# Performance work log

Measured on AMD Instinct MI355X. Metric: run time of the kernel, lower is better.

## Reference

```python
import jax, jax.numpy as jnp
import numpy as np
import math

N_EMBD = 768
N_HEAD = 12
B, T = 4, 1024


def setup_inputs() -> dict:
    key = jax.random.key(0)
    ks = jax.random.split(key, 12)
    s = 0.02
    d = N_EMBD
    inp = {
        'x': jax.random.normal(ks[0], (B, T, d), dtype=jnp.float32),
        'refractory_state': jax.random.uniform(ks[1], (B, T), dtype=jnp.float32),
        'ln1_w': jnp.ones((d,), jnp.float32),
        'ln1_b': jnp.zeros((d,), jnp.float32),
        'c_attn_w': jax.random.normal(ks[2], (d, 3 * d), dtype=jnp.float32) * s,
        'c_attn_b': jnp.zeros((3 * d,), jnp.float32),
        'c_proj_w': jax.random.normal(ks[3], (d, d), dtype=jnp.float32) * s,
        'c_proj_b': jnp.zeros((d,), jnp.float32),
        'threshold': jnp.full((N_HEAD,), 0.01, jnp.float32),
        'leak': jnp.full((N_HEAD,), 2.0, jnp.float32),
        'steepness': jnp.full((N_HEAD,), 2.0, jnp.float32),
        'refractory_strength': jnp.full((N_HEAD,), -2.0, jnp.float32),
        'cross_layer_weight': jnp.full((N_HEAD,), -2.0, jnp.float32),
        'ln2_w': jnp.ones((d,), jnp.float32),
        'ln2_b': jnp.zeros((d,), jnp.float32),
        'fc_w': jax.random.normal(ks[4], (d, 4 * d), dtype=jnp.float32) * s,
        'fc_b': jnp.zeros((4 * d,), jnp.float32),
        'proj_w': jax.random.normal(ks[5], (4 * d, d), dtype=jnp.float32) * s,
        'proj_b': jnp.zeros((d,), jnp.float32),
    }
    return inp


def _layer_norm(x, w, b, eps=1e-5):
    m = jnp.mean(x, axis=-1, keepdims=True)
    v = jnp.var(x, axis=-1, keepdims=True)
    return (x - m) * jax.lax.rsqrt(v + eps) * w + b


def _per_head(p):
    # [H] -> [1, H, 1, 1]
    return p.reshape(1, -1, 1, 1)


def ember_block(x, refractory_state, ln1_w, ln1_b, c_attn_w, c_attn_b,
                c_proj_w, c_proj_b, threshold, leak, steepness,
                refractory_strength, cross_layer_weight,
                ln2_w, ln2_b, fc_w, fc_b, proj_w, proj_b):
    Bx, Tx, C = x.shape
    hd = C // N_HEAD

    h = _layer_norm(x, ln1_w, ln1_b)
    qkv = h @ c_attn_w + c_attn_b
    q, k, v = jnp.split(qkv, 3, axis=-1)
    # [B, T, C] -> [B, H, T, hd]
    q = q.reshape(Bx, Tx, N_HEAD, hd).transpose(0, 2, 1, 3)
    k = k.reshape(Bx, Tx, N_HEAD, hd).transpose(0, 2, 1, 3)
    v = v.reshape(Bx, Tx, N_HEAD, hd).transpose(0, 2, 1, 3)

    att = jnp.einsum('bhqd,bhkd->bhqk', q, k) * (1.0 / math.sqrt(hd))
    causal = jnp.tril(jnp.ones((Tx, Tx), dtype=bool))
    att = jnp.where(causal, att, -jnp.inf)
    att_probs = jax.nn.softmax(att, axis=-1)

    # per-head LIF modulation with refractory dynamics
    thr = jnp.abs(_per_head(threshold)) * 0.1
    lk = jax.nn.sigmoid(_per_head(leak))
    stp = jax.nn.softplus(_per_head(steepness))

    column_load = att_probs.mean(axis=-2, keepdims=True)  # [B,H,1,T]
    ref_strength = jax.nn.softplus(_per_head(refractory_strength))
    eff_thr = thr + ref_strength * column_load
    cross_w = jax.nn.sigmoid(_per_head(cross_layer_weight))
    prev_load = refractory_state[:, None, None, :]  # [B,1,1,T]
    eff_thr = eff_thr + cross_w * prev_load

    fire_mask = jax.nn.sigmoid(stp * (att_probs - eff_thr))
    lif_weights = fire_mask + lk * (1.0 - fire_mask)
    modulated = att_probs * lif_weights
    modulated = modulated / (modulated.sum(axis=-1, keepdims=True) + 1e-8)
    new_refractory = modulated.mean(axis=1).mean(axis=-2)  # [B,T]

    y = jnp.einsum('bhqk,bhkd->bhqd', modulated, v)
    y = y.transpose(0, 2, 1, 3).reshape(Bx, Tx, C)
    y = y @ c_proj_w + c_proj_b
    x = x + y

    # MLP
    h2 = _layer_norm(x, ln2_w, ln2_b)
    h2 = jax.nn.gelu(h2 @ fc_w + fc_b, approximate=False)
    h2 = h2 @ proj_w + proj_b
    x = x + h2
    return x, new_refractory


def reference(x, refractory_state, ln1_w, ln1_b, c_attn_w, c_attn_b,
              c_proj_w, c_proj_b, threshold, leak, steepness,
              refractory_strength, cross_layer_weight,
              ln2_w, ln2_b, fc_w, fc_b, proj_w, proj_b):
    return ember_block(x, refractory_state, ln1_w, ln1_b, c_attn_w, c_attn_b,
                       c_proj_w, c_proj_b, threshold, leak, steepness,
                       refractory_strength, cross_layer_weight,
                       ln2_w, ln2_b, fc_w, fc_b, proj_w, proj_b)
```

## Files before the change

kernel.cpp:

```cpp
#include <hip/hip_runtime.h>
#include <hip/hip_bf16.h>
#include <math.h>

typedef unsigned short ushort;
typedef __attribute__((ext_vector_type(8))) unsigned short ushort8;
typedef __attribute__((ext_vector_type(8))) short s16x8;
typedef __attribute__((ext_vector_type(4))) float f32x4;

constexpr int NE = 768;
constexpr int NH = 12;
constexpr int HD = 64;
constexpr int Bc = 4;
constexpr int Tc = 1024;
constexpr int BT = Bc * Tc;

__device__ __forceinline__ ushort f2bf(float f) {
    __hip_bfloat16 h = __float2bfloat16(f);
    return *reinterpret_cast<ushort*>(&h);
}
__device__ __forceinline__ float bf2f(ushort u) {
    return __uint_as_float(((unsigned)u) << 16);
}
__device__ __forceinline__ float softplus_f(float x) {
    return (x > 20.f) ? x : log1pf(__expf(x));
}
__device__ __forceinline__ float rcp_f(float x) {
#if __has_builtin(__builtin_amdgcn_rcpf)
    return __builtin_amdgcn_rcpf(x);
#else
    return 1.f / x;
#endif
}
__device__ __forceinline__ void gload16(const void* g, void* l) {
    __builtin_amdgcn_global_load_lds((const __attribute__((address_space(1))) void*)g,
                                     (__attribute__((address_space(3))) void*)l, 16, 0, 0);
}

__global__ __launch_bounds__(256) void ln_kernel(const float* __restrict__ x,
                                                 const float* __restrict__ w,
                                                 const float* __restrict__ b,
                                                 ushort* __restrict__ out) {
    int row = blockIdx.x;
    const float* xr = x + (size_t)row * NE;
    int t = threadIdx.x;
    float v0 = xr[t], v1 = xr[t + 256], v2 = xr[t + 512];
    __shared__ float red[256], red2[256];
    red[t] = v0 + v1 + v2;
    red2[t] = v0 * v0 + v1 * v1 + v2 * v2;
    __syncthreads();
    for (int o = 128; o > 0; o >>= 1) {
        if (t < o) { red[t] += red[t + o]; red2[t] += red2[t + o]; }
        __syncthreads();
    }
    float mean = red[0] * (1.0f / NE);
    float var = red2[0] * (1.0f / NE) - mean * mean;
    float rs = rsqrtf(var + 1e-5f);
    ushort* orow = out + (size_t)row * NE;
    orow[t]       = f2bf((v0 - mean) * rs * w[t]       + b[t]);
    orow[t + 256] = f2bf((v1 - mean) * rs * w[t + 256] + b[t + 256]);
    orow[t + 512] = f2bf((v2 - mean) * rs * w[t + 512] + b[t + 512]);
}

__global__ __launch_bounds__(256) void wconvert(const float* __restrict__ W,
                                                ushort* __restrict__ Wt, int K, int N) {
    __shared__ float t[32][33];
    int n0 = blockIdx.x * 32, k0 = blockIdx.y * 32;
    int c = threadIdx.x & 31, r4 = threadIdx.x >> 5;
#pragma unroll
    for (int i = 0; i < 4; ++i) {
        int r = r4 + i * 8;
        t[r][c] = W[(size_t)(k0 + r) * N + n0 + c];
    }
    __syncthreads();
#pragma unroll
    for (int i = 0; i < 4; ++i) {
        int r = r4 + i * 8;
        Wt[(size_t)(n0 + r) * K + k0 + c] = f2bf(t[c][r]);
    }
}

template <int BM, int BN, int OUT_MODE, int ACT, bool RES>
__global__ __launch_bounds__(256) void mfma_gemm(
    const ushort* __restrict__ A, const ushort* __restrict__ Bt,
    const float* __restrict__ bias, const float* __restrict__ residual,
    float* __restrict__ Cf, ushort* __restrict__ Cb,
    ushort* __restrict__ Qo, ushort* __restrict__ Ko, ushort* __restrict__ Vo,
    int M, int N, int K, int NBX) {
    constexpr int NF = (BM == 128) ? 4 : 2;
    constexpr int MF = (BM == 64 && BN == 64) ? 2 : 4;
    constexpr int WN = BN / (NF * 16);
    constexpr int APASS = BM / 32, BPASS = BN / 32;
    __shared__ __align__(16) ushort As[BM * 64];
    __shared__ __align__(16) ushort Bs[BN * 64];
    int tid = threadIdx.x;
    int lane = tid & 63;
    int nb = gridDim.x;
    int lin = blockIdx.x;
    int nl = (lin & 7) * (nb >> 3) + (lin >> 3);
    int bx = nl % NBX, by = nl / NBX;
    int m0 = by * BM, n0 = bx * BN;
    int wave = tid >> 6;
    int wr = wave / WN, wc = wave % WN;
    f32x4 acc[MF][NF] = {};
    int srow = tid >> 3;
    int scol = (tid & 7) ^ (srow & 7);
    const ushort* ga = A + (size_t)(m0 + srow) * K + scol * 8;
    const ushort* gb = Bt + (size_t)(n0 + srow) * K + scol * 8;
    char* lA = (char*)As + tid * 16;
    char* lB = (char*)Bs + tid * 16;
    int fr = lane & 15, g = lane >> 4;
    unsigned swz = (unsigned)((fr & 7) << 4);
    const char* abase = (const char*)As + (wr * (MF * 16) + fr) * 128;
    const char* bbase = (const char*)Bs + (wc * (NF * 16) + fr) * 128;
    for (int k0 = 0; k0 < K; k0 += 64) {
#pragma unroll
        for (int p = 0; p < APASS; ++p)
            gload16(ga + (size_t)(p * 32) * K + k0, lA + p * 4096);
#pragma unroll
        for (int p = 0; p < BPASS; ++p)
            gload16(gb + (size_t)(p * 32) * K + k0, lB + p * 4096);
        __syncthreads();
#pragma unroll
        for (int ks = 0; ks < 2; ++ks) {
            unsigned o = ((unsigned)(g * 16 + ks * 64)) ^ swz;
            s16x8 af[MF], bf[NF];
#pragma unroll
            for (int i = 0; i < MF; ++i) af[i] = *(const s16x8*)(abase + i * 2048 + o);
#pragma unroll
            for (int i = 0; i < NF; ++i) bf[i] = *(const s16x8*)(bbase + i * 2048 + o);
#pragma unroll
            for (int mi = 0; mi < MF; ++mi)
#pragma unroll
                for (int ni = 0; ni < NF; ++ni)
                    acc[mi][ni] = __builtin_amdgcn_mfma_f32_16x16x32_bf16(af[mi], bf[ni], acc[mi][ni], 0, 0, 0);
        }
        __syncthreads();
    }
#pragma unroll
    for (int mi = 0; mi < MF; ++mi) {
#pragma unroll
        for (int ni = 0; ni < NF; ++ni) {
#pragma unroll
            for (int j = 0; j < 4; ++j) {
                int row = m0 + wr * (MF * 16) + mi * 16 + g * 4 + j;
                int col = n0 + wc * (NF * 16) + ni * 16 + fr;
                float v = acc[mi][ni][j] + bias[col];
                if (ACT == 1) v = 0.5f * v * (1.0f + erff(v * 0.70710678118654752f));
                if (RES) v += residual[(size_t)row * N + col];
                if (OUT_MODE == 0) {
                    Cf[(size_t)row * N + col] = v;
                } else if (OUT_MODE == 1) {
                    Cb[(size_t)row * N + col] = f2bf(v);
                } else {
                    int which = col >= 1536 ? 2 : (col >= 768 ? 1 : 0);
                    int rem = col - which * 768;
                    int hh = rem >> 6, d = rem & 63;
                    int b_ = row >> 10, t_ = row & 1023;
                    if (which == 2)
                        Vo[((size_t)(b_ * NH + hh) * HD + d) * Tc + t_] = f2bf(v);
                    else {
                        ushort* dst = which == 0 ? Qo : Ko;
                        dst[((size_t)(b_ * NH + hh) * Tc + t_) * HD + d] = f2bf(v);
                    }
                }
            }
        }
    }
}


__global__ __launch_bounds__(256) void attn_P(
    const ushort* __restrict__ Qp, const ushort* __restrict__ Kp,
    ushort* __restrict__ Pbuf, float* __restrict__ denom, float* __restrict__ colsum) {
    int beta = blockIdx.x;
    int tq = 63 - beta / 48;
    int bh = beta % 48;
    int tid = threadIdx.x;
    int w = tid >> 6, lane = tid & 63, qlane = lane & 15, g = lane >> 4;
    __shared__ ushort plds[4][16][48];
    __shared__ float cs[1056];
    __shared__ float dden[4][16];
    __shared__ float dinvL[16];
    int nst = (tq + 2) >> 1;
    int base = nst >> 2, rem = nst & 3;
    int slo = w * base + (w < rem ? w : rem);
    int shi = slo + base + (w < rem ? 1 : 0);
    int kmaxc = (tq + 1) * 16;
    for (int i = tid; i < 1056; i += 256) cs[i] = 0.f;
    const ushort* Qb = Qp + (size_t)bh * Tc * HD;
    const ushort* Kb = Kp + (size_t)bh * Tc * HD;
    const ushort* qr = Qb + (size_t)(tq * 16 + qlane) * HD + g * 8;
    s16x8 qf0 = *(const s16x8*)qr;
    s16x8 qf1 = *(const s16x8*)(qr + 32);
    ushort* panel = Pbuf + ((size_t)bh * 1056 + (unsigned)(((tq + 1) * (tq + 1)) >> 2)) * 512;
    int q = tq * 16 + qlane;
    float dpart = 0.f;
    for (int s = slo; s < shi; ++s) {
        int kt0 = 2 * s, kt1 = 2 * s + 1;
        {
            const ushort* kr = Kb + (size_t)(kt0 * 16 + qlane) * HD + g * 8;
            s16x8 kf0 = *(const s16x8*)kr;
            s16x8 kf1 = *(const s16x8*)(kr + 32);
            f32x4 z = {0.f, 0.f, 0.f, 0.f};
            z = __builtin_amdgcn_mfma_f32_16x16x32_bf16(kf0, qf0, z, 0, 0, 0);
            z = __builtin_amdgcn_mfma_f32_16x16x32_bf16(kf1, qf1, z, 0, 0, 0);
#pragma unroll
            for (int j = 0; j < 4; ++j) {
                int key = kt0 * 16 + g * 4 + j;
                float p = (key <= q) ? __expf(z[j] * 0.125f - 8.f) : 0.f;
                dpart += p;
                plds[w][qlane][g * 4 + j] = f2bf(p);
            }
        }
        if (kt1 <= tq) {
            const ushort* kr = Kb + (size_t)(kt1 * 16 + qlane) * HD + g * 8;
            s16x8 kf0 = *(const s16x8*)kr;
            s16x8 kf1 = *(const s16x8*)(kr + 32);
            f32x4 z = {0.f, 0.f, 0.f, 0.f};
            z = __builtin_amdgcn_mfma_f32_16x16x32_bf16(kf0, qf0, z, 0, 0, 0);
            z = __builtin_amdgcn_mfma_f32_16x16x32_bf16(kf1, qf1, z, 0, 0, 0);
#pragma unroll
            for (int j = 0; j < 4; ++j) {
                int key = kt1 * 16 + g * 4 + j;
                float p = (key <= q) ? __expf(z[j] * 0.125f - 8.f) : 0.f;
                dpart += p;
                plds[w][qlane][16 + g * 4 + j] = f2bf(p);
            }
        } else {
#pragma unroll
            for (int j = 0; j < 4; ++j) plds[w][qlane][16 + g * 4 + j] = 0;
        }
        s16x8 pa = *(const s16x8*)&plds[w][qlane][g * 8];
        *(s16x8*)(panel + (size_t)s * 512 + lane * 8) = pa;
    }
    dpart += __shfl_xor(dpart, 16);
    dpart += __shfl_xor(dpart, 32);
    if (lane < 16) dden[w][lane] = dpart;
    __syncthreads();
    if (tid < 16) {
        float d = dden[0][tid] + dden[1][tid] + dden[2][tid] + dden[3][tid];
        denom[(size_t)bh * Tc + tq * 16 + tid] = d;
        dinvL[tid] = rcp_f(d);
    }
    __syncthreads();
    float dinvq = dinvL[qlane];
    for (int s = slo; s < shi; ++s) {
        s16x8 v8 = *(const s16x8*)(panel + (size_t)s * 512 + lane * 8);
        int k0 = s * 32 + g * 8;
#pragma unroll
        for (int j = 0; j < 8; ++j) {
            float r = bf2f((ushort)v8[j]) * dinvq;
            r += __shfl_xor(r, 1);
            r += __shfl_xor(r, 2);
            r += __shfl_xor(r, 4);
            r += __shfl_xor(r, 8);
            if (qlane == 0) cs[k0 + j] += r;
        }
    }
    __syncthreads();
    for (int i = tid; i < kmaxc; i += 256)
        atomicAdd(&colsum[(size_t)bh * Tc + i], cs[i]);
}

__global__ __launch_bounds__(256) void attn_CD(
    const ushort* __restrict__ Pbuf, const ushort* __restrict__ Vt,
    const float* __restrict__ denom, const float* __restrict__ colsum,
    const float* __restrict__ refr_in,
    const float* __restrict__ threshold, const float* __restrict__ leak,
    const float* __restrict__ steepness, const float* __restrict__ refr_strength,
    const float* __restrict__ cross_w,
    ushort* __restrict__ ybuf, float* __restrict__ refr_out) {
    int beta = blockIdx.x;
    int tq = 63 - beta / 48;
    int bh = beta % 48;
    int b = bh / NH, h = bh - b * NH;
    int tid = threadIdx.x;
    int w = tid >> 6, lane = tid & 63, qlane = lane & 15, g = lane >> 4;
    __shared__ float eff[1056];
    __shared__ float cs[1056];
    __shared__ float msum[4][16];
    __shared__ float minvL[16];
    __shared__ float ylds[16][64];
    int nst = (tq + 2) >> 1;
    int base = nst >> 2, rem = nst & 3;
    int slo = w * base + (w < rem ? w : rem);
    int shi = slo + base + (w < rem ? 1 : 0);
    int kmaxc = (tq + 1) * 16;
    float thr = fabsf(threshold[h]) * 0.1f;
    float lk = 1.f / (1.f + __expf(-leak[h]));
    float lk1m = 1.f - lk;
    float stp = softplus_f(steepness[h]);
    float rfs = softplus_f(refr_strength[h]);
    float crw = 1.f / (1.f + __expf(-cross_w[h]));
    for (int i = tid; i < 1056; i += 256) {
        eff[i] = (i < kmaxc)
                     ? thr + rfs * (colsum[(size_t)bh * Tc + i] * (1.f / 1024.f))
                           + crw * refr_in[(size_t)b * Tc + i]
                     : 0.f;
        cs[i] = 0.f;
    }
    for (int i = tid; i < 1024; i += 256) ((float*)ylds)[i] = 0.f;
    float dinvq = rcp_f(denom[(size_t)bh * Tc + tq * 16 + qlane]);
    __syncthreads();
    const ushort* panel =
        Pbuf + ((size_t)bh * 1056 + (unsigned)(((tq + 1) * (tq + 1)) >> 2)) * 512;
    float msp = 0.f;
#pragma unroll 2
    for (int s = slo; s < shi; ++s) {
        s16x8 v8 = *(const s16x8*)(panel + (size_t)s * 512 + lane * 8);
        int k0 = s * 32 + g * 8;
#pragma unroll
        for (int j = 0; j < 8; ++j) {
            float p = bf2f((ushort)v8[j]) * dinvq;
            float fire = rcp_f(1.f + __expf(-stp * (p - eff[k0 + j])));
            msp += p * (lk + lk1m * fire);
        }
    }
    msp += __shfl_xor(msp, 16);
    msp += __shfl_xor(msp, 32);
    if (lane < 16) msum[w][lane] = msp;
    __syncthreads();
    if (tid < 16)
        minvL[tid] = rcp_f(msum[0][tid] + msum[1][tid] + msum[2][tid] + msum[3][tid] + 1e-8f);
    __syncthreads();
    float minvq = minvL[qlane];
    const ushort* Vh = Vt + (size_t)bh * HD * Tc;
    f32x4 accY[4] = {};
    for (int s = slo; s < shi; ++s) {
        s16x8 v8 = *(const s16x8*)(panel + (size_t)s * 512 + lane * 8);
        int k0 = s * 32 + g * 8;
        s16x8 pa;
#pragma unroll
        for (int j = 0; j < 8; ++j) {
            float p = bf2f((ushort)v8[j]) * dinvq;
            float fire = rcp_f(1.f + __expf(-stp * (p - eff[k0 + j])));
            float pt = p * (lk + lk1m * fire);
            pa[j] = (short)f2bf(pt);
            float r = pt * minvq;
            r += __shfl_xor(r, 1);
            r += __shfl_xor(r, 2);
            r += __shfl_xor(r, 4);
            r += __shfl_xor(r, 8);
            if (qlane == 0) cs[k0 + j] += r;
        }
#pragma unroll
        for (int dt = 0; dt < 4; ++dt) {
            const ushort* vp = Vh + (size_t)(dt * 16 + qlane) * Tc + s * 32 + g * 8;
            s16x8 vf = *(const s16x8*)vp;
            accY[dt] = __builtin_amdgcn_mfma_f32_16x16x32_bf16(pa, vf, accY[dt], 0, 0, 0);
        }
    }
#pragma unroll
    for (int dt = 0; dt < 4; ++dt)
#pragma unroll
        for (int j = 0; j < 4; ++j)
            atomicAdd(&ylds[g * 4 + j][dt * 16 + qlane], accY[dt][j]);
    __syncthreads();
    for (int i = tid; i < 1024; i += 256) {
        int qq = i >> 6, dd = i & 63;
        ybuf[(size_t)(b * Tc + tq * 16 + qq) * NE + h * 64 + dd] =
            f2bf(ylds[qq][dd] * minvL[qq]);
    }
    for (int i = tid; i < kmaxc; i += 256)
        atomicAdd(&refr_out[(size_t)b * Tc + i], cs[i] * (1.f / (NH * Tc)));
}

extern "C" void kernel_launch(void* const* d_in, const int* in_sizes, int n_in,
                              void* d_out, int out_size, void* d_ws, size_t ws_size,
                              hipStream_t stream) {
    const float* x        = (const float*)d_in[0];
    const float* refr     = (const float*)d_in[1];
    const float* ln1_w    = (const float*)d_in[2];
    const float* ln1_b    = (const float*)d_in[3];
    const float* c_attn_w = (const float*)d_in[4];
    const float* c_attn_b = (const float*)d_in[5];
    const float* c_proj_w = (const float*)d_in[6];
    const float* c_proj_b = (const float*)d_in[7];
    const float* threshold = (const float*)d_in[8];
    const float* leak      = (const float*)d_in[9];
    const float* steepness = (const float*)d_in[10];
    const float* refractory_strength = (const float*)d_in[11];
    const float* cross_layer_weight  = (const float*)d_in[12];
    const float* ln2_w    = (const float*)d_in[13];
    const float* ln2_b    = (const float*)d_in[14];
    const float* fc_w     = (const float*)d_in[15];
    const float* fc_b     = (const float*)d_in[16];
    const float* proj_w   = (const float*)d_in[17];
    const float* proj_b   = (const float*)d_in[18];

    char* ws = (char*)d_ws;
    ushort* hbuf   = (ushort*)(ws + 0);
    ushort* qb     = (ushort*)(ws + 6291456);
    ushort* kb     = (ushort*)(ws + 12582912);
    ushort* vtg    = (ushort*)(ws + 18874368);
    ushort* ybuf   = (ushort*)(ws + 25165824);
    ushort* fc_act = (ushort*)(ws + 6291456);
    float*  denomb = (float*)(ws + 31457280);
    float*  colsum = (float*)(ws + 31653888);
    ushort* wt_attn  = (ushort*)(ws + 31850496);
    ushort* wt_cproj = (ushort*)(ws + 35389440);
    ushort* wt_fc    = (ushort*)(ws + 36569088);
    ushort* wt_proj  = (ushort*)(ws + 41287680);
    ushort* Pbuf     = (ushort*)(ws + 46006272);

    float* xout = (float*)d_out;
    float* refr_out = xout + (size_t)BT * NE;

    hipMemsetAsync(colsum, 0, (size_t)Bc * NH * Tc * sizeof(float), stream);
    hipMemsetAsync(refr_out, 0, (size_t)Bc * Tc * sizeof(float), stream);

    wconvert<<<dim3(2304 / 32, 768 / 32), 256, 0, stream>>>(c_attn_w, wt_attn, 768, 2304);
    wconvert<<<dim3(768 / 32, 768 / 32), 256, 0, stream>>>(c_proj_w, wt_cproj, 768, 768);
    wconvert<<<dim3(3072 / 32, 768 / 32), 256, 0, stream>>>(fc_w, wt_fc, 768, 3072);
    wconvert<<<dim3(768 / 32, 3072 / 32), 256, 0, stream>>>(proj_w, wt_proj, 3072, 768);

    ln_kernel<<<BT, 256, 0, stream>>>(x, ln1_w, ln1_b, hbuf);

    mfma_gemm<64, 128, 2, 0, false><<<1152, 256, 0, stream>>>(
        hbuf, wt_attn, c_attn_b, nullptr, nullptr, nullptr, qb, kb, vtg,
        BT, 3 * NE, NE, 18);

    attn_P<<<48 * 64, 256, 0, stream>>>(qb, kb, Pbuf, denomb, colsum);
    attn_CD<<<48 * 64, 256, 0, stream>>>(
        Pbuf, vtg, denomb, colsum, refr, threshold, leak, steepness,
        refractory_strength, cross_layer_weight, ybuf, refr_out);

    mfma_gemm<64, 64, 0, 0, true><<<768, 256, 0, stream>>>(
        ybuf, wt_cproj, c_proj_b, x, xout, nullptr, nullptr, nullptr, nullptr,
        BT, NE, NE, 12);

    ln_kernel<<<BT, 256, 0, stream>>>(xout, ln2_w, ln2_b, hbuf);

    mfma_gemm<128, 128, 1, 1, false><<<768, 256, 0, stream>>>(
        hbuf, wt_fc, fc_b, nullptr, nullptr, fc_act, nullptr, nullptr, nullptr,
        BT, 4 * NE, NE, 24);

    mfma_gemm<64, 64, 0, 0, true><<<768, 256, 0, stream>>>(
        fc_act, wt_proj, proj_b, xout, xout, nullptr, nullptr, nullptr, nullptr,
        BT, NE, 4 * NE, 12);
}
```

Before: 297.0 us.

## Pair causal query tiles per block and double-buffer small GEMM tiles

The attention kernels now process two query tiles per block, a long one (63-qp) paired with a short one (qp), so every block handles 33 key strips. That balances the causal triangle and halves the grid. attn_CD keeps the modulated probabilities in registers between the two passes instead of re-reading the panel, and switches shared-memory column sums to atomics. The 64x64 GEMMs get LDS double buffering with explicit vmcnt waits, so global loads overlap MFMA work, at the cost of more registers and LDS.

```diff
diff --git a/kernel.cpp b/kernel.cpp
--- a/kernel.cpp
+++ b/kernel.cpp
@@ -90,8 +90,10 @@
     constexpr int MF = (BM == 64 && BN == 64) ? 2 : 4;
     constexpr int WN = BN / (NF * 16);
     constexpr int APASS = BM / 32, BPASS = BN / 32;
-    __shared__ __align__(16) ushort As[BM * 64];
-    __shared__ __align__(16) ushort Bs[BN * 64];
+    constexpr bool DBUF = (BM == 64 && BN == 64);
+    constexpr int NBUF = DBUF ? 2 : 1;
+    __shared__ __align__(16) ushort As[NBUF * BM * 64];
+    __shared__ __align__(16) ushort Bs[NBUF * BN * 64];
     int tid = threadIdx.x;
     int lane = tid & 63;
     int nb = gridDim.x;
@@ -112,29 +114,74 @@
     unsigned swz = (unsigned)((fr & 7) << 4);
     const char* abase = (const char*)As + (wr * (MF * 16) + fr) * 128;
     const char* bbase = (const char*)Bs + (wc * (NF * 16) + fr) * 128;
-    for (int k0 = 0; k0 < K; k0 += 64) {
-#pragma unroll
-        for (int p = 0; p < APASS; ++p)
-            gload16(ga + (size_t)(p * 32) * K + k0, lA + p * 4096);
-#pragma unroll
-        for (int p = 0; p < BPASS; ++p)
-            gload16(gb + (size_t)(p * 32) * K + k0, lB + p * 4096);
-        __syncthreads();
-#pragma unroll
-        for (int ks = 0; ks < 2; ++ks) {
-            unsigned o = ((unsigned)(g * 16 + ks * 64)) ^ swz;
-            s16x8 af[MF], bf[NF];
-#pragma unroll
-            for (int i = 0; i < MF; ++i) af[i] = *(const s16x8*)(abase + i * 2048 + o);
-#pragma unroll
-            for (int i = 0; i < NF; ++i) bf[i] = *(const s16x8*)(bbase + i * 2048 + o);
-#pragma unroll
-            for (int mi = 0; mi < MF; ++mi)
-#pragma unroll
-                for (int ni = 0; ni < NF; ++ni)
-                    acc[mi][ni] = __builtin_amdgcn_mfma_f32_16x16x32_bf16(af[mi], bf[ni], acc[mi][ni], 0, 0, 0);
-        }
-        __syncthreads();
+
+    if constexpr (DBUF) {
+        constexpr int ABYTES = BM * 64 * 2, BBYTES = BN * 64 * 2;
+        int nk = K >> 6;
+#pragma unroll
+        for (int p = 0; p < APASS; ++p) gload16(ga + (size_t)(p * 32) * K, lA + p * 4096);
+#pragma unroll
+        for (int p = 0; p < BPASS; ++p) gload16(gb + (size_t)(p * 32) * K, lB + p * 4096);
+        for (int k = 0; k < nk; ++k) {
+            int cur = k & 1;
+            if (k + 1 < nk) {
+                int nxt = cur ^ 1;
+                int k0 = (k + 1) << 6;
+#pragma unroll
+                for (int p = 0; p < APASS; ++p)
+                    gload16(ga + (size_t)(p * 32) * K + k0, lA + nxt * ABYTES + p * 4096);
+#pragma unroll
+                for (int p = 0; p < BPASS; ++p)
+                    gload16(gb + (size_t)(p * 32) * K + k0, lB + nxt * BBYTES + p * 4096);
+                asm volatile("s_waitcnt vmcnt(4)" ::: "memory");
+            } else {
+                asm volatile("s_waitcnt vmcnt(0)" ::: "memory");
+            }
+            __builtin_amdgcn_s_barrier();
+#pragma unroll
+            for (int ks = 0; ks < 2; ++ks) {
+                unsigned o = ((unsigned)(g * 16 + ks * 64)) ^ swz;
+                s16x8 af[MF], bf[NF];
+#pragma unroll
+                for (int i = 0; i < MF; ++i)
+                    af[i] = *(const s16x8*)(abase + cur * ABYTES + i * 2048 + o);
+#pragma unroll
+                for (int i = 0; i < NF; ++i)
+                    bf[i] = *(const s16x8*)(bbase + cur * BBYTES + i * 2048 + o);
+#pragma unroll
+                for (int mi = 0; mi < MF; ++mi)
+#pragma unroll
+                    for (int ni = 0; ni < NF; ++ni)
+                        acc[mi][ni] = __builtin_amdgcn_mfma_f32_16x16x32_bf16(af[mi], bf[ni], acc[mi][ni], 0, 0, 0);
+            }
+            asm volatile("s_waitcnt lgkmcnt(0)" ::: "memory");
+            __builtin_amdgcn_s_barrier();
+        }
+    } else {
+        for (int k0 = 0; k0 < K; k0 += 64) {
+#pragma unroll
+            for (int p = 0; p < APASS; ++p)
+                gload16(ga + (size_t)(p * 32) * K + k0, lA + p * 4096);
+#pragma unroll
+            for (int p = 0; p < BPASS; ++p)
+                gload16(gb + (size_t)(p * 32) * K + k0, lB + p * 4096);
+            __syncthreads();
+#pragma unroll
+            for (int ks = 0; ks < 2; ++ks) {
+                unsigned o = ((unsigned)(g * 16 + ks * 64)) ^ swz;
+                s16x8 af[MF], bf[NF];
+#pragma unroll
+                for (int i = 0; i < MF; ++i) af[i] = *(const s16x8*)(abase + i * 2048 + o);
+#pragma unroll
+                for (int i = 0; i < NF; ++i) bf[i] = *(const s16x8*)(bbase + i * 2048 + o);
+#pragma unroll
+                for (int mi = 0; mi < MF; ++mi)
+#pragma unroll
+                    for (int ni = 0; ni < NF; ++ni)
+                        acc[mi][ni] = __builtin_amdgcn_mfma_f32_16x16x32_bf16(af[mi], bf[ni], acc[mi][ni], 0, 0, 0);
+            }
+            __syncthreads();
+        }
     }
 #pragma unroll
     for (int mi = 0; mi < MF; ++mi) {
@@ -172,31 +219,38 @@
 __global__ __launch_bounds__(256) void attn_P(
     const ushort* __restrict__ Qp, const ushort* __restrict__ Kp,
     ushort* __restrict__ Pbuf, float* __restrict__ denom, float* __restrict__ colsum) {
-    int beta = blockIdx.x;
-    int tq = 63 - beta / 48;
-    int bh = beta % 48;
+    int bid = blockIdx.x;
+    int bh = bid % 48, qp = bid / 48;
+    int ta = 63 - qp, tb = qp;
+    int nst_a = (ta + 2) >> 1;
     int tid = threadIdx.x;
     int w = tid >> 6, lane = tid & 63, qlane = lane & 15, g = lane >> 4;
-    __shared__ ushort plds[4][16][48];
+    __shared__ __align__(16) ushort plds[4][16][40];
     __shared__ float cs[1056];
-    __shared__ float dden[4][16];
-    __shared__ float dinvL[16];
-    int nst = (tq + 2) >> 1;
-    int base = nst >> 2, rem = nst & 3;
-    int slo = w * base + (w < rem ? w : rem);
-    int shi = slo + base + (w < rem ? 1 : 0);
-    int kmaxc = (tq + 1) * 16;
+    __shared__ float dden[4][2][16];
+    __shared__ float dinvL[2][16];
+    int kmax_a = (ta + 1) * 16;
     for (int i = tid; i < 1056; i += 256) cs[i] = 0.f;
     const ushort* Qb = Qp + (size_t)bh * Tc * HD;
     const ushort* Kb = Kp + (size_t)bh * Tc * HD;
-    const ushort* qr = Qb + (size_t)(tq * 16 + qlane) * HD + g * 8;
-    s16x8 qf0 = *(const s16x8*)qr;
-    s16x8 qf1 = *(const s16x8*)(qr + 32);
-    ushort* panel = Pbuf + ((size_t)bh * 1056 + (unsigned)(((tq + 1) * (tq + 1)) >> 2)) * 512;
-    int q = tq * 16 + qlane;
-    float dpart = 0.f;
-    for (int s = slo; s < shi; ++s) {
+    const ushort* qra = Qb + (size_t)(ta * 16 + qlane) * HD + g * 8;
+    const ushort* qrb = Qb + (size_t)(tb * 16 + qlane) * HD + g * 8;
+    s16x8 qa0 = *(const s16x8*)qra, qa1 = *(const s16x8*)(qra + 32);
+    s16x8 qb0 = *(const s16x8*)qrb, qb1 = *(const s16x8*)(qrb + 32);
+    ushort* panA = Pbuf + ((size_t)bh * 1056 + (unsigned)(((ta + 1) * (ta + 1)) >> 2)) * 512;
+    ushort* panB = Pbuf + ((size_t)bh * 1056 + (unsigned)(((tb + 1) * (tb + 1)) >> 2)) * 512;
+    int slo = (w * 33) >> 2, shi = ((w + 1) * 33) >> 2;
+    float dpa = 0.f, dpb = 0.f;
+    for (int sig = slo; sig < shi; ++sig) {
+        bool isA = sig < nst_a;
+        int s = isA ? sig : sig - nst_a;
+        int t = isA ? ta : tb;
+        s16x8 qf0 = isA ? qa0 : qb0;
+        s16x8 qf1 = isA ? qa1 : qb1;
+        ushort* panel = isA ? panA : panB;
+        int q = t * 16 + qlane;
         int kt0 = 2 * s, kt1 = 2 * s + 1;
+        float dloc = 0.f;
         {
             const ushort* kr = Kb + (size_t)(kt0 * 16 + qlane) * HD + g * 8;
             s16x8 kf0 = *(const s16x8*)kr;
@@ -208,11 +262,11 @@
             for (int j = 0; j < 4; ++j) {
                 int key = kt0 * 16 + g * 4 + j;
                 float p = (key <= q) ? __expf(z[j] * 0.125f - 8.f) : 0.f;
-                dpart += p;
+                dloc += p;
                 plds[w][qlane][g * 4 + j] = f2bf(p);
             }
         }
-        if (kt1 <= tq) {
+        if (kt1 <= t) {
             const ushort* kr = Kb + (size_t)(kt1 * 16 + qlane) * HD + g * 8;
             s16x8 kf0 = *(const s16x8*)kr;
             s16x8 kf1 = *(const s16x8*)(kr + 32);
@@ -223,7 +277,7 @@
             for (int j = 0; j < 4; ++j) {
                 int key = kt1 * 16 + g * 4 + j;
                 float p = (key <= q) ? __expf(z[j] * 0.125f - 8.f) : 0.f;
-                dpart += p;
+                dloc += p;
                 plds[w][qlane][16 + g * 4 + j] = f2bf(p);
             }
         } else {
@@ -232,19 +286,28 @@
         }
         s16x8 pa = *(const s16x8*)&plds[w][qlane][g * 8];
         *(s16x8*)(panel + (size_t)s * 512 + lane * 8) = pa;
-    }
-    dpart += __shfl_xor(dpart, 16);
-    dpart += __shfl_xor(dpart, 32);
-    if (lane < 16) dden[w][lane] = dpart;
-    __syncthreads();
-    if (tid < 16) {
-        float d = dden[0][tid] + dden[1][tid] + dden[2][tid] + dden[3][tid];
-        denom[(size_t)bh * Tc + tq * 16 + tid] = d;
-        dinvL[tid] = rcp_f(d);
-    }
-    __syncthreads();
-    float dinvq = dinvL[qlane];
-    for (int s = slo; s < shi; ++s) {
+        if (isA) dpa += dloc; else dpb += dloc;
+    }
+    dpa += __shfl_xor(dpa, 16);
+    dpa += __shfl_xor(dpa, 32);
+    dpb += __shfl_xor(dpb, 16);
+    dpb += __shfl_xor(dpb, 32);
+    if (lane < 16) { dden[w][0][lane] = dpa; dden[w][1][lane] = dpb; }
+    __syncthreads();
+    if (tid < 32) {
+        int t_ = tid >> 4, l = tid & 15;
+        float d = dden[0][t_][l] + dden[1][t_][l] + dden[2][t_][l] + dden[3][t_][l];
+        int tt = t_ ? tb : ta;
+        denom[(size_t)bh * Tc + tt * 16 + l] = d;
+        dinvL[t_][l] = rcp_f(d);
+    }
+    __syncthreads();
+    float dia = dinvL[0][qlane], dib = dinvL[1][qlane];
+    for (int sig = slo; sig < shi; ++sig) {
+        bool isA = sig < nst_a;
+        int s = isA ? sig : sig - nst_a;
+        const ushort* panel = isA ? panA : panB;
+        float dinvq = isA ? dia : dib;
         s16x8 v8 = *(const s16x8*)(panel + (size_t)s * 512 + lane * 8);
         int k0 = s * 32 + g * 8;
 #pragma unroll
@@ -254,11 +317,11 @@
             r += __shfl_xor(r, 2);
             r += __shfl_xor(r, 4);
             r += __shfl_xor(r, 8);
-            if (qlane == 0) cs[k0 + j] += r;
-        }
-    }
-    __syncthreads();
-    for (int i = tid; i < kmaxc; i += 256)
+            if (qlane == 0) atomicAdd(&cs[k0 + j], r);
+        }
+    }
+    __syncthreads();
+    for (int i = tid; i < kmax_a; i += 256)
         atomicAdd(&colsum[(size_t)bh * Tc + i], cs[i]);
 }
 
@@ -270,22 +333,19 @@
     const float* __restrict__ steepness, const float* __restrict__ refr_strength,
     const float* __restrict__ cross_w,
     ushort* __restrict__ ybuf, float* __restrict__ refr_out) {
-    int beta = blockIdx.x;
-    int tq = 63 - beta / 48;
-    int bh = beta % 48;
+    int bid = blockIdx.x;
+    int bh = bid % 48, qp = bid / 48;
+    int ta = 63 - qp, tb = qp;
+    int nst_a = (ta + 2) >> 1;
     int b = bh / NH, h = bh - b * NH;
     int tid = threadIdx.x;
     int w = tid >> 6, lane = tid & 63, qlane = lane & 15, g = lane >> 4;
     __shared__ float eff[1056];
     __shared__ float cs[1056];
-    __shared__ float msum[4][16];
-    __shared__ float minvL[16];
-    __shared__ float ylds[16][64];
-    int nst = (tq + 2) >> 1;
-    int base = nst >> 2, rem = nst & 3;
-    int slo = w * base + (w < rem ? w : rem);
-    int shi = slo + base + (w < rem ? 1 : 0);
-    int kmaxc = (tq + 1) * 16;
+    __shared__ float msum[4][2][16];
+    __shared__ float minvL[2][16];
+    __shared__ float ylds[2][16][64];
+    int kmax_a = (ta + 1) * 16;
     float thr = fabsf(threshold[h]) * 0.1f;
     float lk = 1.f / (1.f + __expf(-leak[h]));
     float lk1m = 1.f - lk;
@@ -293,75 +353,117 @@
     float rfs = softplus_f(refr_strength[h]);
     float crw = 1.f / (1.f + __expf(-cross_w[h]));
     for (int i = tid; i < 1056; i += 256) {
-        eff[i] = (i < kmaxc)
+        eff[i] = (i < kmax_a)
                      ? thr + rfs * (colsum[(size_t)bh * Tc + i] * (1.f / 1024.f))
                            + crw * refr_in[(size_t)b * Tc + i]
                      : 0.f;
         cs[i] = 0.f;
     }
-    for (int i = tid; i < 1024; i += 256) ((float*)ylds)[i] = 0.f;
-    float dinvq = rcp_f(denom[(size_t)bh * Tc + tq * 16 + qlane]);
-    __syncthreads();
-    const ushort* panel =
-        Pbuf + ((size_t)bh * 1056 + (unsigned)(((tq + 1) * (tq + 1)) >> 2)) * 512;
-    float msp = 0.f;
-#pragma unroll 2
-    for (int s = slo; s < shi; ++s) {
-        s16x8 v8 = *(const s16x8*)(panel + (size_t)s * 512 + lane * 8);
-        int k0 = s * 32 + g * 8;
-#pragma unroll
-        for (int j = 0; j < 8; ++j) {
-            float p = bf2f((ushort)v8[j]) * dinvq;
-            float fire = rcp_f(1.f + __expf(-stp * (p - eff[k0 + j])));
-            msp += p * (lk + lk1m * fire);
-        }
-    }
-    msp += __shfl_xor(msp, 16);
-    msp += __shfl_xor(msp, 32);
-    if (lane < 16) msum[w][lane] = msp;
-    __syncthreads();
-    if (tid < 16)
-        minvL[tid] = rcp_f(msum[0][tid] + msum[1][tid] + msum[2][tid] + msum[3][tid] + 1e-8f);
-    __syncthreads();
-    float minvq = minvL[qlane];
+    for (int i = tid; i < 2048; i += 256) ((float*)ylds)[i] = 0.f;
+    float dinva = rcp_f(denom[(size_t)bh * Tc + ta * 16 + qlane]);
+    float dinvb = rcp_f(denom[(size_t)bh * Tc + tb * 16 + qlane]);
+    __syncthreads();
+    const ushort* panA =
+        Pbuf + ((size_t)bh * 1056 + (unsigned)(((ta + 1) * (ta + 1)) >> 2)) * 512;
+    const ushort* panB =
+        Pbuf + ((size_t)bh * 1056 + (unsigned)(((tb + 1) * (tb + 1)) >> 2)) * 512;
+    int slo = (w * 33) >> 2, shi = ((w + 1) * 33) >> 2;
+    s16x8 ptreg[9];
+    float mspa = 0.f, mspb = 0.f;
+#pragma unroll
+    for (int u = 0; u < 9; ++u) {
+        int sig = slo + u;
+        if (sig < shi) {
+            bool isA = sig < nst_a;
+            int s = isA ? sig : sig - nst_a;
+            const ushort* panel = isA ? panA : panB;
+            float dinvq = isA ? dinva : dinvb;
+            s16x8 v8 = *(const s16x8*)(panel + (size_t)s * 512 + lane * 8);
+            int k0 = s * 32 + g * 8;
+            s16x8 pw;
+            float mloc = 0.f;
+#pragma unroll
+            for (int j = 0; j < 8; ++j) {
+                float p = bf2f((ushort)v8[j]) * dinvq;
+                float fire = rcp_f(1.f + __expf(-stp * (p - eff[k0 + j])));
+                float pt = p * (lk + lk1m * fire);
+                mloc += pt;
+                pw[j] = (short)f2bf(pt);
+            }
+            ptreg[u] = pw;
+            if (isA) mspa += mloc; else mspb += mloc;
+        }
+    }
+    mspa += __shfl_xor(mspa, 16);
+    mspa += __shfl_xor(mspa, 32);
+    mspb += __shfl_xor(mspb, 16);
+    mspb += __shfl_xor(mspb, 32);
+    if (lane < 16) { msum[w][0][lane] = mspa; msum[w][1][lane] = mspb; }
+    __syncthreads();
+    if (tid < 32) {
+        int t_ = tid >> 4, l = tid & 15;
+        minvL[t_][l] = rcp_f(msum[0][t_][l] + msum[1][t_][l] + msum[2][t_][l] +
+                             msum[3][t_][l] + 1e-8f);
+    }
+    __syncthreads();
+    float minva = minvL[0][qlane], minvb = minvL[1][qlane];
     const ushort* Vh = Vt + (size_t)bh * HD * Tc;
     f32x4 accY[4] = {};
-    for (int s = slo; s < shi; ++s) {
-        s16x8 v8 = *(const s16x8*)(panel + (size_t)s * 512 + lane * 8);
-        int k0 = s * 32 + g * 8;
-        s16x8 pa;
-#pragma unroll
-        for (int j = 0; j < 8; ++j) {
-            float p = bf2f((ushort)v8[j]) * dinvq;
-            float fire = rcp_f(1.f + __expf(-stp * (p - eff[k0 + j])));
-            float pt = p * (lk + lk1m * fire);
-            pa[j] = (short)f2bf(pt);
-            float r = pt * minvq;
-            r += __shfl_xor(r, 1);
-            r += __shfl_xor(r, 2);
-            r += __shfl_xor(r, 4);
-            r += __shfl_xor(r, 8);
-            if (qlane == 0) cs[k0 + j] += r;
-        }
-#pragma unroll
-        for (int dt = 0; dt < 4; ++dt) {
-            const ushort* vp = Vh + (size_t)(dt * 16 + qlane) * Tc + s * 32 + g * 8;
-            s16x8 vf = *(const s16x8*)vp;
-            accY[dt] = __builtin_amdgcn_mfma_f32_16x16x32_bf16(pa, vf, accY[dt], 0, 0, 0);
-        }
-    }
-#pragma unroll
-    for (int dt = 0; dt < 4; ++dt)
-#pragma unroll
-        for (int j = 0; j < 4; ++j)
-            atomicAdd(&ylds[g * 4 + j][dt * 16 + qlane], accY[dt][j]);
-    __syncthreads();
-    for (int i = tid; i < 1024; i += 256) {
-        int qq = i >> 6, dd = i & 63;
-        ybuf[(size_t)(b * Tc + tq * 16 + qq) * NE + h * 64 + dd] =
-            f2bf(ylds[qq][dd] * minvL[qq]);
-    }
-    for (int i = tid; i < kmaxc; i += 256)
+    int curT = -1;
+#pragma unroll
+    for (int u = 0; u < 9; ++u) {
+        int sig = slo + u;
+        if (sig < shi) {
+            bool isA = sig < nst_a;
+            int t_ = isA ? 0 : 1;
+            int s = isA ? sig : sig - nst_a;
+            s16x8 pa = ptreg[u];
+            int k0 = s * 32 + g * 8;
+            float minvq = isA ? minva : minvb;
+#pragma unroll
+            for (int j = 0; j < 8; ++j) {
+                float r = bf2f((ushort)pa[j]) * minvq;
+                r += __shfl_xor(r, 1);
+                r += __shfl_xor(r, 2);
+                r += __shfl_xor(r, 4);
+                r += __shfl_xor(r, 8);
+                if (qlane == 0) atomicAdd(&cs[k0 + j], r);
+            }
+            if (t_ != curT) {
+                if (curT >= 0) {
+#pragma unroll
+                    for (int dt = 0; dt < 4; ++dt)
+#pragma unroll
+                        for (int j = 0; j < 4; ++j) {
+                            atomicAdd(&ylds[curT][g * 4 + j][dt * 16 + qlane], accY[dt][j]);
+                            accY[dt][j] = 0.f;
+                        }
+                }
+                curT = t_;
+            }
+#pragma unroll
+            for (int dt = 0; dt < 4; ++dt) {
+                const ushort* vp = Vh + (size_t)(dt * 16 + qlane) * Tc + s * 32 + g * 8;
+                s16x8 vf = *(const s16x8*)vp;
+                accY[dt] = __builtin_amdgcn_mfma_f32_16x16x32_bf16(pa, vf, accY[dt], 0, 0, 0);
+            }
+        }
+    }
+    if (curT >= 0) {
+#pragma unroll
+        for (int dt = 0; dt < 4; ++dt)
+#pragma unroll
+            for (int j = 0; j < 4; ++j)
+                atomicAdd(&ylds[curT][g * 4 + j][dt * 16 + qlane], accY[dt][j]);
+    }
+    __syncthreads();
+    for (int i = tid; i < 2048; i += 256) {
+        int t_ = i >> 10, q = (i >> 6) & 15, d = i & 63;
+        int tt = t_ ? tb : ta;
+        ybuf[(size_t)(b * Tc + tt * 16 + q) * NE + h * 64 + d] =
+            f2bf(ylds[t_][q][d] * minvL[t_][q]);
+    }
+    for (int i = tid; i < kmax_a; i += 256)
         atomicAdd(&refr_out[(size_t)b * Tc + i], cs[i] * (1.f / (NH * Tc)));
 }
 
@@ -420,8 +522,8 @@
         hbuf, wt_attn, c_attn_b, nullptr, nullptr, nullptr, qb, kb, vtg,
         BT, 3 * NE, NE, 18);
 
-    attn_P<<<48 * 64, 256, 0, stream>>>(qb, kb, Pbuf, denomb, colsum);
-    attn_CD<<<48 * 64, 256, 0, stream>>>(
+    attn_P<<<48 * 32, 256, 0, stream>>>(qb, kb, Pbuf, denomb, colsum);
+    attn_CD<<<48 * 32, 256, 0, stream>>>(
         Pbuf, vtg, denomb, colsum, refr, threshold, leak, steepness,
         refractory_strength, cross_layer_weight, ybuf, refr_out);
 
```

After: 294.0 us. No clear change (-1.0%).
